# Performance work log

Measured on AMD Instinct MI355X. Metric: run time of the kernel, lower is better.

## Reference

```python
import jax, jax.numpy as jnp
import numpy as np

EMBED_DIM = 1024
NUM_HEADS = 16
HEAD_DIM = EMBED_DIM // NUM_HEADS


def setup_inputs() -> dict:
    key = jax.random.key(0)
    kx, kw1, kb1, kw2, kb2 = jax.random.split(key, 5)
    B, T, C = 4, 2048, EMBED_DIM
    s = 1.0 / np.sqrt(C)
    return {
        "x": jax.random.normal(kx, (B, T, C), dtype=jnp.float32),
        "qkv_w": jax.random.uniform(kw1, (3 * C, C), jnp.float32, -s, s),
        "qkv_b": jax.random.uniform(kb1, (3 * C,), jnp.float32, -s, s),
        "out_w": jax.random.uniform(kw2, (C, C), jnp.float32, -s, s),
        "out_b": jax.random.uniform(kb2, (C,), jnp.float32, -s, s),
    }


def reference(x, qkv_w, qkv_b, out_w, out_b):
    B, T, C = x.shape
    H, D = NUM_HEADS, HEAD_DIM
    qkv = x @ qkv_w.T + qkv_b                      # [B,T,3C]
    qkv = qkv.reshape(B, T, 3, H, D)
    q = qkv[:, :, 0].transpose(0, 2, 1, 3)         # [B,H,T,D]
    k = qkv[:, :, 1].transpose(0, 2, 1, 3)
    v = qkv[:, :, 2].transpose(0, 2, 1, 3)
    att = jnp.einsum("bhqd,bhkd->bhqk", q, k) / jnp.sqrt(jnp.float32(D))
    causal = jnp.tril(jnp.ones((T, T), dtype=bool))
    att = jnp.where(causal, att, -jnp.inf)
    att = jax.nn.softmax(att, axis=-1)
    out = jnp.einsum("bhqk,bhkd->bhqd", att, v)    # [B,H,T,D]
    out = out.transpose(0, 2, 1, 3).reshape(B, T, C)
    return out @ out_w.T + out_b
```

## Files before the change

### kernel.cpp

```cpp
#include <hip/hip_runtime.h>
#include <stdint.h>

typedef _Float16 f16;
typedef _Float16 f16x2 __attribute__((ext_vector_type(2)));
typedef _Float16 f16x4 __attribute__((ext_vector_type(4)));
typedef _Float16 f16x8 __attribute__((ext_vector_type(8)));
typedef float f32x4 __attribute__((ext_vector_type(4)));

#define LOG2E 1.44269504088896340736f

__device__ __forceinline__ f32x4 mfma_16x16x32(f16x8 a, f16x8 b, f32x4 c) {
    return __builtin_amdgcn_mfma_f32_16x16x32_f16(a, b, c, 0, 0, 0);
}

__device__ __forceinline__ void gload_lds16(const void* g, void* l) {
    __builtin_amdgcn_global_load_lds(
        (const __attribute__((address_space(1))) unsigned int*)g,
        (__attribute__((address_space(3))) unsigned int*)l, 16, 0, 0);
}

__device__ __forceinline__ f16x2 cvt_pk_f16(float a, float b) {
    return __builtin_bit_cast(f16x2, __builtin_amdgcn_cvt_pkrtz(a, b));
}

__global__ void cast_f32_f16(const float* __restrict__ src, f16* __restrict__ dst, int n4) {
    int i = blockIdx.x * 256 + threadIdx.x;
    if (i >= n4) return;
    float4 v = reinterpret_cast<const float4*>(src)[i];
    f16x4 o;
    o[0] = (f16)v.x; o[1] = (f16)v.y; o[2] = (f16)v.z; o[3] = (f16)v.w;
    reinterpret_cast<f16x4*>(dst)[i] = o;
}

template<int MODE>
__global__ __launch_bounds__(256, 2)
void gemm_tn(const f16* __restrict__ A, const f16* __restrict__ W,
             const float* __restrict__ bias, void* __restrict__ outp,
             int M, int N, int K)
{
    __shared__ __align__(16) f16 As[128 * 32];
    __shared__ __align__(16) f16 Bs[128 * 32];

    const int lane = threadIdx.x & 63;
    const int wave = threadIdx.x >> 6;
    const int l15 = lane & 15, l4 = lane >> 4;

    const int nwg = (int)(gridDim.x * gridDim.y);
    int orig = (int)(blockIdx.y * gridDim.x + blockIdx.x);
    int cpx = nwg >> 3;
    int w = (orig & 7) * cpx + (orig >> 3);
    const int row0 = (w / (int)gridDim.x) * 128;
    const int col0 = (w % (int)gridDim.x) * 128;
    const int wr = wave >> 1, wc = wave & 1;

    f32x4 acc[4][4] = {};

    const int srow = lane >> 2;
    const int scol = (lane & 3) * 8;

    for (int k0 = 0; k0 < K; k0 += 32) {
        __syncthreads();
        #pragma unroll
        for (int it = 0; it < 2; ++it) {
            int chunk = it * 4 + wave;
            const f16* gA = A + (size_t)(row0 + chunk * 16 + srow) * K + k0 + scol;
            gload_lds16(gA, As + chunk * 512);
            const f16* gB = W + (size_t)(col0 + chunk * 16 + srow) * K + k0 + scol;
            gload_lds16(gB, Bs + chunk * 512);
        }
        __syncthreads();

        f16x8 af[4], bf[4];
        #pragma unroll
        for (int m = 0; m < 4; ++m)
            af[m] = *reinterpret_cast<const f16x8*>(As + (wr * 64 + m * 16 + l15) * 32 + l4 * 8);
        #pragma unroll
        for (int n = 0; n < 4; ++n)
            bf[n] = *reinterpret_cast<const f16x8*>(Bs + (wc * 64 + n * 16 + l15) * 32 + l4 * 8);
        #pragma unroll
        for (int m = 0; m < 4; ++m)
            #pragma unroll
            for (int n = 0; n < 4; ++n)
                acc[m][n] = mfma_16x16x32(af[m], bf[n], acc[m][n]);
    }

    if (MODE == 0) {
        f16* qb = (f16*)outp;
        const size_t HS = (size_t)64 * 2048 * 64;
        #pragma unroll
        for (int m = 0; m < 4; ++m) {
            int rbase = row0 + wr * 64 + m * 16 + l4 * 4;
            #pragma unroll
            for (int n = 0; n < 4; ++n) {
                int j = col0 + wc * 64 + n * 16 + l15;
                int which = j >> 10;
                int h = (j >> 6) & 15;
                int d = j & 63;
                float bj = bias[j];
                f16* base = qb + (size_t)which * HS;
                float scale = (which == 0) ? (0.125f * LOG2E) : 1.0f;
                #pragma unroll
                for (int r = 0; r < 4; ++r) {
                    int row = rbase + r;
                    int b = row >> 11, t = row & 2047;
                    size_t off = ((size_t)(b * 16 + h) * 2048 + t) * 64 + d;
                    base[off] = (f16)((acc[m][n][r] + bj) * scale);
                }
            }
        }
    } else {
        float* O = (float*)outp;
        #pragma unroll
        for (int m = 0; m < 4; ++m) {
            int rbase = row0 + wr * 64 + m * 16 + l4 * 4;
            #pragma unroll
            for (int n = 0; n < 4; ++n) {
                int j = col0 + wc * 64 + n * 16 + l15;
                float bj = bias[j];
                #pragma unroll
                for (int r = 0; r < 4; ++r)
                    O[(size_t)(rbase + r) * N + j] = acc[m][n][r] + bj;
            }
        }
    }
}

__global__ __launch_bounds__(256, 3)
void attn_kernel(const f16* __restrict__ qb, const f16* __restrict__ kb,
                 const f16* __restrict__ vb, f16* __restrict__ ob)
{
    __shared__ __align__(16) f16 Ks[2][64 * 64];
    __shared__ __align__(16) f16 Vs[2][64][72];
    __shared__ __align__(16) f16 Ps[4][16][72];

    const int tid = (int)threadIdx.x;
    const int bh = (int)blockIdx.x;
    const int qblk = (int)gridDim.y - 1 - (int)blockIdx.y;
    const int lane = tid & 63;
    const int wave = tid >> 6;
    const int l15 = lane & 15, l4 = lane >> 4;
    const int q0 = qblk * 64;
    const int qw = q0 + wave * 16;

    const f16* Qp = qb + ((size_t)bh * 2048 + qw) * 64;
    f16x8 aq0 = *reinterpret_cast<const f16x8*>(Qp + l15 * 64 + l4 * 8);
    f16x8 aq1 = *reinterpret_cast<const f16x8*>(Qp + l15 * 64 + 32 + l4 * 8);

    float Mr = -1e30f, Lr = 0.0f;
    f32x4 oacc[4] = {};

    const int ntiles = q0 / 64 + 1;
    const f16* Kbh = kb + (size_t)bh * 2048 * 64;
    const f16* Vbh = vb + (size_t)bh * 2048 * 64;

    f16x8 vld0, vld1;
    {
        #pragma unroll
        for (int it = 0; it < 2; ++it) {
            int c = it * 256 + tid;
            int krow = c >> 3;
            int s16 = (c & 7) ^ (krow & 7);
            gload_lds16(Kbh + krow * 64 + s16 * 8, &Ks[0][0] + it * 2048 + wave * 512);
        }
        vld0 = *reinterpret_cast<const f16x8*>(Vbh + lane * 64 + (wave * 2 + 0) * 8);
        vld1 = *reinterpret_cast<const f16x8*>(Vbh + lane * 64 + (wave * 2 + 1) * 8);
    }

    for (int t = 0; t < ntiles; ++t) {
        const int cur = t & 1;

        #pragma unroll
        for (int it = 0; it < 2; ++it) {
            int dblk = wave * 2 + it;
            const f16x8 v = it ? vld1 : vld0;
            #pragma unroll
            for (int e = 0; e < 8; ++e)
                Vs[cur][dblk * 8 + e][lane] = v[e];
        }

        __syncthreads();

        {
            const int kvn = (t + 1 < ntiles) ? (t + 1) * 64 : t * 64;
            const f16* Ktn = Kbh + (size_t)kvn * 64;
            #pragma unroll
            for (int it = 0; it < 2; ++it) {
                int c = it * 256 + tid;
                int krow = c >> 3;
                int s16 = (c & 7) ^ (krow & 7);
                gload_lds16(Ktn + krow * 64 + s16 * 8, &Ks[cur ^ 1][0] + it * 2048 + wave * 512);
            }
            const f16* Vtn = Vbh + (size_t)kvn * 64;
            vld0 = *reinterpret_cast<const f16x8*>(Vtn + lane * 64 + (wave * 2 + 0) * 8);
            vld1 = *reinterpret_cast<const f16x8*>(Vtn + lane * 64 + (wave * 2 + 1) * 8);
        }

        f32x4 s[4];
        __builtin_amdgcn_s_setprio(1);
        #pragma unroll
        for (int n = 0; n < 4; ++n) {
            int key = n * 16 + l15;
            int cs = key & 7;
            f16x8 kf0 = *reinterpret_cast<const f16x8*>(&Ks[cur][0] + key * 64 + ((l4 ^ cs) * 8));
            f16x8 kf1 = *reinterpret_cast<const f16x8*>(&Ks[cur][0] + key * 64 + (((4 + l4) ^ cs) * 8));
            f32x4 c = {};
            c = mfma_16x16x32(kf0, aq0, c);
            c = mfma_16x16x32(kf1, aq1, c);
            s[n] = c;
        }
        __builtin_amdgcn_s_setprio(0);

        if (t == ntiles - 1) {
            #pragma unroll
            for (int n = 0; n < 4; ++n)
                #pragma unroll
                for (int r = 0; r < 4; ++r)
                    if (n * 16 + l4 * 4 + r > wave * 16 + l15) s[n][r] = -1e30f;
        }

        float mx = -1e30f;
        #pragma unroll
        for (int n = 0; n < 4; ++n)
            #pragma unroll
            for (int r = 0; r < 4; ++r)
                mx = fmaxf(mx, s[n][r]);
        mx = fmaxf(mx, __shfl_xor(mx, 16));
        mx = fmaxf(mx, __shfl_xor(mx, 32));

        if (__any(mx > Mr + 8.0f)) {
            float nm = fmaxf(Mr, mx);
            float alpha = exp2f(Mr - nm);
            Mr = nm;
            float ar[4];
            #pragma unroll
            for (int r = 0; r < 4; ++r) ar[r] = __shfl(alpha, l4 * 4 + r);
            #pragma unroll
            for (int dt = 0; dt < 4; ++dt) {
                oacc[dt][0] *= ar[0]; oacc[dt][1] *= ar[1];
                oacc[dt][2] *= ar[2]; oacc[dt][3] *= ar[3];
            }
            Lr *= alpha;
        }

        float rs = 0.0f;
        #pragma unroll
        for (int n = 0; n < 4; ++n) {
            float p0 = exp2f(s[n][0] - Mr);
            float p1 = exp2f(s[n][1] - Mr);
            float p2 = exp2f(s[n][2] - Mr);
            float p3 = exp2f(s[n][3] - Mr);
            rs += (p0 + p1) + (p2 + p3);
            f16x2 lo = cvt_pk_f16(p0, p1);
            f16x2 hi = cvt_pk_f16(p2, p3);
            f16x4 pk; pk[0] = lo[0]; pk[1] = lo[1]; pk[2] = hi[0]; pk[3] = hi[1];
            *reinterpret_cast<f16x4*>(&Ps[wave][l15][n * 16 + l4 * 4]) = pk;
        }
        rs += __shfl_xor(rs, 16);
        rs += __shfl_xor(rs, 32);
        Lr += rs;

        f16x8 pa0 = *reinterpret_cast<const f16x8*>(&Ps[wave][l15][l4 * 8]);
        f16x8 pa1 = *reinterpret_cast<const f16x8*>(&Ps[wave][l15][32 + l4 * 8]);
        __builtin_amdgcn_s_setprio(1);
        #pragma unroll
        for (int dt = 0; dt < 4; ++dt) {
            int d = dt * 16 + l15;
            f16x8 v0 = *reinterpret_cast<const f16x8*>(&Vs[cur][d][l4 * 8]);
            f16x8 v1 = *reinterpret_cast<const f16x8*>(&Vs[cur][d][32 + l4 * 8]);
            oacc[dt] = mfma_16x16x32(pa0, v0, oacc[dt]);
            oacc[dt] = mfma_16x16x32(pa1, v1, oacc[dt]);
        }
        __builtin_amdgcn_s_setprio(0);
    }

    float lr[4];
    #pragma unroll
    for (int r = 0; r < 4; ++r) lr[r] = __shfl(Lr, l4 * 4 + r);

    const int b = bh >> 4, h = bh & 15;
    f16* O = ob + ((size_t)b * 2048 + qw) * 1024 + h * 64;
    #pragma unroll
    for (int dt = 0; dt < 4; ++dt) {
        int d = dt * 16 + l15;
        #pragma unroll
        for (int r = 0; r < 4; ++r)
            O[(size_t)(l4 * 4 + r) * 1024 + d] = (f16)(oacc[dt][r] / lr[r]);
    }
}

extern "C" void kernel_launch(void* const* d_in, const int* in_sizes, int n_in,
                              void* d_out, int out_size, void* d_ws, size_t ws_size,
                              hipStream_t stream)
{
    const float* x    = (const float*)d_in[0];
    const float* qkvw = (const float*)d_in[1];
    const float* qkvb = (const float*)d_in[2];
    const float* outw = (const float*)d_in[3];
    const float* outb = (const float*)d_in[4];
    float* out = (float*)d_out;

    f16* x_h    = (f16*)d_ws;
    f16* qkvw_h = x_h + (size_t)8192 * 1024;
    f16* outw_h = qkvw_h + (size_t)3072 * 1024;
    f16* q_buf  = outw_h + (size_t)1024 * 1024;
    f16* att_o  = q_buf + (size_t)3 * 8388608;

    cast_f32_f16<<<8192, 256, 0, stream>>>(x, x_h, 2097152);
    cast_f32_f16<<<3072, 256, 0, stream>>>(qkvw, qkvw_h, 786432);
    cast_f32_f16<<<1024, 256, 0, stream>>>(outw, outw_h, 262144);

    gemm_tn<0><<<dim3(24, 64), 256, 0, stream>>>(x_h, qkvw_h, qkvb, q_buf, 8192, 3072, 1024);
    attn_kernel<<<dim3(64, 32), 256, 0, stream>>>(q_buf, q_buf + 8388608, q_buf + 2 * 8388608, att_o);
    gemm_tn<1><<<dim3(8, 64), 256, 0, stream>>>(att_o, outw_h, outb, out, 8192, 1024, 1024);
}
```

Baseline: 198.3 us.

## Use 32x32 MFMA with 128-query tiles in causal attention kernel

The attention kernel now handles 128 query rows per block (32 per wave) with 32x32x16 MFMA tiles in place of 16x16x32. Each K/V tile loaded into LDS is therefore reused by twice as many queries, and the grid shrinks to half as many blocks. Waves whose queries lie entirely before a K/V tile skip its compute, and the K LDS layout changes to a chunked, unswizzled arrangement. The costs are fewer blocks for occupancy, more registers for the 16-wide accumulators, and possible LDS bank conflicts from the new padding.

```diff
diff --git a/kernel.cpp b/kernel.cpp
--- a/kernel.cpp
+++ b/kernel.cpp
@@ -6,11 +6,15 @@
 typedef _Float16 f16x4 __attribute__((ext_vector_type(4)));
 typedef _Float16 f16x8 __attribute__((ext_vector_type(8)));
 typedef float f32x4 __attribute__((ext_vector_type(4)));
+typedef float f32x16 __attribute__((ext_vector_type(16)));
 
 #define LOG2E 1.44269504088896340736f
 
 __device__ __forceinline__ f32x4 mfma_16x16x32(f16x8 a, f16x8 b, f32x4 c) {
     return __builtin_amdgcn_mfma_f32_16x16x32_f16(a, b, c, 0, 0, 0);
+}
+__device__ __forceinline__ f32x16 mfma_32x32x16(f16x8 a, f16x8 b, f32x16 c) {
+    return __builtin_amdgcn_mfma_f32_32x32x16_f16(a, b, c, 0, 0, 0);
 }
 
 __device__ __forceinline__ void gload_lds16(const void* g, void* l) {
@@ -129,27 +133,30 @@
 void attn_kernel(const f16* __restrict__ qb, const f16* __restrict__ kb,
                  const f16* __restrict__ vb, f16* __restrict__ ob)
 {
-    __shared__ __align__(16) f16 Ks[2][64 * 64];
-    __shared__ __align__(16) f16 Vs[2][64][72];
-    __shared__ __align__(16) f16 Ps[4][16][72];
+    __shared__ __align__(16) f16 Ks[2][4096];
+    __shared__ __align__(16) f16 Vs[2][64][68];
+    __shared__ __align__(16) f16 Ps[4][32][68];
 
     const int tid = (int)threadIdx.x;
     const int bh = (int)blockIdx.x;
     const int qblk = (int)gridDim.y - 1 - (int)blockIdx.y;
     const int lane = tid & 63;
     const int wave = tid >> 6;
-    const int l15 = lane & 15, l4 = lane >> 4;
-    const int q0 = qblk * 64;
-    const int qw = q0 + wave * 16;
+    const int l31 = lane & 31;
+    const int hi  = lane >> 5;
+    const int q0 = qblk * 128;
+    const int qw = q0 + wave * 32;
 
     const f16* Qp = qb + ((size_t)bh * 2048 + qw) * 64;
-    f16x8 aq0 = *reinterpret_cast<const f16x8*>(Qp + l15 * 64 + l4 * 8);
-    f16x8 aq1 = *reinterpret_cast<const f16x8*>(Qp + l15 * 64 + 32 + l4 * 8);
+    f16x8 qf[4];
+    #pragma unroll
+    for (int ss = 0; ss < 4; ++ss)
+        qf[ss] = *reinterpret_cast<const f16x8*>(Qp + l31 * 64 + ss * 16 + hi * 8);
 
     float Mr = -1e30f, Lr = 0.0f;
-    f32x4 oacc[4] = {};
-
-    const int ntiles = q0 / 64 + 1;
+    f32x16 oacc[2] = {};
+
+    const int ntiles = 2 * qblk + 2;
     const f16* Kbh = kb + (size_t)bh * 2048 * 64;
     const f16* Vbh = vb + (size_t)bh * 2048 * 64;
 
@@ -157,10 +164,8 @@
     {
         #pragma unroll
         for (int it = 0; it < 2; ++it) {
-            int c = it * 256 + tid;
-            int krow = c >> 3;
-            int s16 = (c & 7) ^ (krow & 7);
-            gload_lds16(Kbh + krow * 64 + s16 * 8, &Ks[0][0] + it * 2048 + wave * 512);
+            int c = it * 4 + wave;
+            gload_lds16(Kbh + lane * 64 + c * 8, &Ks[0][0] + c * 512);
         }
         vld0 = *reinterpret_cast<const f16x8*>(Vbh + lane * 64 + (wave * 2 + 0) * 8);
         vld1 = *reinterpret_cast<const f16x8*>(Vbh + lane * 64 + (wave * 2 + 1) * 8);
@@ -168,6 +173,7 @@
 
     for (int t = 0; t < ntiles; ++t) {
         const int cur = t & 1;
+        const int kv0 = t * 64;
 
         #pragma unroll
         for (int it = 0; it < 2; ++it) {
@@ -185,107 +191,124 @@
             const f16* Ktn = Kbh + (size_t)kvn * 64;
             #pragma unroll
             for (int it = 0; it < 2; ++it) {
-                int c = it * 256 + tid;
-                int krow = c >> 3;
-                int s16 = (c & 7) ^ (krow & 7);
-                gload_lds16(Ktn + krow * 64 + s16 * 8, &Ks[cur ^ 1][0] + it * 2048 + wave * 512);
+                int c = it * 4 + wave;
+                gload_lds16(Ktn + lane * 64 + c * 8, &Ks[cur ^ 1][0] + c * 512);
             }
             const f16* Vtn = Vbh + (size_t)kvn * 64;
             vld0 = *reinterpret_cast<const f16x8*>(Vtn + lane * 64 + (wave * 2 + 0) * 8);
             vld1 = *reinterpret_cast<const f16x8*>(Vtn + lane * 64 + (wave * 2 + 1) * 8);
         }
 
-        f32x4 s[4];
-        __builtin_amdgcn_s_setprio(1);
-        #pragma unroll
-        for (int n = 0; n < 4; ++n) {
-            int key = n * 16 + l15;
-            int cs = key & 7;
-            f16x8 kf0 = *reinterpret_cast<const f16x8*>(&Ks[cur][0] + key * 64 + ((l4 ^ cs) * 8));
-            f16x8 kf1 = *reinterpret_cast<const f16x8*>(&Ks[cur][0] + key * 64 + (((4 + l4) ^ cs) * 8));
-            f32x4 c = {};
-            c = mfma_16x16x32(kf0, aq0, c);
-            c = mfma_16x16x32(kf1, aq1, c);
-            s[n] = c;
-        }
-        __builtin_amdgcn_s_setprio(0);
-
-        if (t == ntiles - 1) {
-            #pragma unroll
-            for (int n = 0; n < 4; ++n)
-                #pragma unroll
-                for (int r = 0; r < 4; ++r)
-                    if (n * 16 + l4 * 4 + r > wave * 16 + l15) s[n][r] = -1e30f;
-        }
-
-        float mx = -1e30f;
-        #pragma unroll
-        for (int n = 0; n < 4; ++n)
-            #pragma unroll
-            for (int r = 0; r < 4; ++r)
-                mx = fmaxf(mx, s[n][r]);
-        mx = fmaxf(mx, __shfl_xor(mx, 16));
-        mx = fmaxf(mx, __shfl_xor(mx, 32));
-
-        if (__any(mx > Mr + 8.0f)) {
-            float nm = fmaxf(Mr, mx);
-            float alpha = exp2f(Mr - nm);
-            Mr = nm;
-            float ar[4];
-            #pragma unroll
-            for (int r = 0; r < 4; ++r) ar[r] = __shfl(alpha, l4 * 4 + r);
-            #pragma unroll
-            for (int dt = 0; dt < 4; ++dt) {
-                oacc[dt][0] *= ar[0]; oacc[dt][1] *= ar[1];
-                oacc[dt][2] *= ar[2]; oacc[dt][3] *= ar[3];
-            }
-            Lr *= alpha;
-        }
-
-        float rs = 0.0f;
-        #pragma unroll
-        for (int n = 0; n < 4; ++n) {
-            float p0 = exp2f(s[n][0] - Mr);
-            float p1 = exp2f(s[n][1] - Mr);
-            float p2 = exp2f(s[n][2] - Mr);
-            float p3 = exp2f(s[n][3] - Mr);
-            rs += (p0 + p1) + (p2 + p3);
-            f16x2 lo = cvt_pk_f16(p0, p1);
-            f16x2 hi = cvt_pk_f16(p2, p3);
-            f16x4 pk; pk[0] = lo[0]; pk[1] = lo[1]; pk[2] = hi[0]; pk[3] = hi[1];
-            *reinterpret_cast<f16x4*>(&Ps[wave][l15][n * 16 + l4 * 4]) = pk;
-        }
-        rs += __shfl_xor(rs, 16);
-        rs += __shfl_xor(rs, 32);
-        Lr += rs;
-
-        f16x8 pa0 = *reinterpret_cast<const f16x8*>(&Ps[wave][l15][l4 * 8]);
-        f16x8 pa1 = *reinterpret_cast<const f16x8*>(&Ps[wave][l15][32 + l4 * 8]);
-        __builtin_amdgcn_s_setprio(1);
-        #pragma unroll
-        for (int dt = 0; dt < 4; ++dt) {
-            int d = dt * 16 + l15;
-            f16x8 v0 = *reinterpret_cast<const f16x8*>(&Vs[cur][d][l4 * 8]);
-            f16x8 v1 = *reinterpret_cast<const f16x8*>(&Vs[cur][d][32 + l4 * 8]);
-            oacc[dt] = mfma_16x16x32(pa0, v0, oacc[dt]);
-            oacc[dt] = mfma_16x16x32(pa1, v1, oacc[dt]);
-        }
-        __builtin_amdgcn_s_setprio(0);
+        if (kv0 <= qw + 31) {
+            const f16* Ksc = &Ks[cur][0];
+
+            f32x16 s0 = {}, s1 = {};
+            __builtin_amdgcn_s_setprio(1);
+            #pragma unroll
+            for (int ss = 0; ss < 4; ++ss) {
+                f16x8 kf0 = *reinterpret_cast<const f16x8*>(Ksc + (2 * ss + hi) * 512 + l31 * 8);
+                f16x8 kf1 = *reinterpret_cast<const f16x8*>(Ksc + (2 * ss + hi) * 512 + (32 + l31) * 8);
+                s0 = mfma_32x32x16(kf0, qf[ss], s0);
+                s1 = mfma_32x32x16(kf1, qf[ss], s1);
+            }
+            __builtin_amdgcn_s_setprio(0);
+
+            if (kv0 + 63 > qw) {
+                const int qg = qw + l31;
+                #pragma unroll
+                for (int r = 0; r < 16; ++r) {
+                    int k0g = kv0 + (r & 3) + 8 * (r >> 2) + 4 * hi;
+                    if (k0g > qg)      s0[r] = -1e30f;
+                    if (k0g + 32 > qg) s1[r] = -1e30f;
+                }
+            }
+
+            float t16[16];
+            #pragma unroll
+            for (int i = 0; i < 16; ++i) t16[i] = fmaxf(s0[i], s1[i]);
+            #pragma unroll
+            for (int st = 8; st > 0; st >>= 1)
+                #pragma unroll
+                for (int i = 0; i < st; ++i) t16[i] = fmaxf(t16[i], t16[i + st]);
+            float mx = t16[0];
+            mx = fmaxf(mx, __shfl_xor(mx, 32));
+
+            if (__any(mx > Mr + 8.0f)) {
+                float nm = fmaxf(Mr, mx);
+                float alpha = exp2f(Mr - nm);
+                Mr = nm; Lr *= alpha;
+                float ar[16];
+                #pragma unroll
+                for (int r = 0; r < 16; ++r)
+                    ar[r] = __shfl(alpha, (r & 3) + 8 * (r >> 2) + 4 * hi);
+                #pragma unroll
+                for (int r = 0; r < 16; ++r) { oacc[0][r] *= ar[r]; oacc[1][r] *= ar[r]; }
+            }
+
+            float e0[16], e1[16];
+            #pragma unroll
+            for (int r = 0; r < 16; ++r) {
+                e0[r] = exp2f(s0[r] - Mr);
+                e1[r] = exp2f(s1[r] - Mr);
+            }
+            float sm[16];
+            #pragma unroll
+            for (int i = 0; i < 16; ++i) sm[i] = e0[i] + e1[i];
+            #pragma unroll
+            for (int st = 8; st > 0; st >>= 1)
+                #pragma unroll
+                for (int i = 0; i < st; ++i) sm[i] += sm[i + st];
+            float rs = sm[0];
+            rs += __shfl_xor(rs, 32);
+            Lr += rs;
+
+            f16* Pw = &Ps[wave][l31][0];
+            #pragma unroll
+            for (int w = 0; w < 4; ++w) {
+                f16x2 lo0 = cvt_pk_f16(e0[4 * w],     e0[4 * w + 1]);
+                f16x2 hi0 = cvt_pk_f16(e0[4 * w + 2], e0[4 * w + 3]);
+                f16x4 p4; p4[0] = lo0[0]; p4[1] = lo0[1]; p4[2] = hi0[0]; p4[3] = hi0[1];
+                *reinterpret_cast<f16x4*>(Pw + 8 * w + 4 * hi) = p4;
+                f16x2 lo1 = cvt_pk_f16(e1[4 * w],     e1[4 * w + 1]);
+                f16x2 hi1 = cvt_pk_f16(e1[4 * w + 2], e1[4 * w + 3]);
+                f16x4 q4; q4[0] = lo1[0]; q4[1] = lo1[1]; q4[2] = hi1[0]; q4[3] = hi1[1];
+                *reinterpret_cast<f16x4*>(Pw + 32 + 8 * w + 4 * hi) = q4;
+            }
+
+            __builtin_amdgcn_s_setprio(1);
+            #pragma unroll
+            for (int ss = 0; ss < 4; ++ss) {
+                f16x4 a0 = *reinterpret_cast<const f16x4*>(Pw + 16 * ss + 8 * hi);
+                f16x4 a1 = *reinterpret_cast<const f16x4*>(Pw + 16 * ss + 8 * hi + 4);
+                f16x8 pa = __builtin_shufflevector(a0, a1, 0, 1, 2, 3, 4, 5, 6, 7);
+                #pragma unroll
+                for (int db = 0; db < 2; ++db) {
+                    const f16* vp = &Vs[cur][db * 32 + l31][16 * ss + 8 * hi];
+                    f16x4 v0 = *reinterpret_cast<const f16x4*>(vp);
+                    f16x4 v1 = *reinterpret_cast<const f16x4*>(vp + 4);
+                    f16x8 vf = __builtin_shufflevector(v0, v1, 0, 1, 2, 3, 4, 5, 6, 7);
+                    oacc[db] = mfma_32x32x16(pa, vf, oacc[db]);
+                }
+            }
+            __builtin_amdgcn_s_setprio(0);
+        }
     }
 
-    float lr[4];
+    float rcp = 1.0f / Lr;
+    float rr[16];
     #pragma unroll
-    for (int r = 0; r < 4; ++r) lr[r] = __shfl(Lr, l4 * 4 + r);
+    for (int r = 0; r < 16; ++r)
+        rr[r] = __shfl(rcp, (r & 3) + 8 * (r >> 2) + 4 * hi);
 
     const int b = bh >> 4, h = bh & 15;
     f16* O = ob + ((size_t)b * 2048 + qw) * 1024 + h * 64;
     #pragma unroll
-    for (int dt = 0; dt < 4; ++dt) {
-        int d = dt * 16 + l15;
-        #pragma unroll
-        for (int r = 0; r < 4; ++r)
-            O[(size_t)(l4 * 4 + r) * 1024 + d] = (f16)(oacc[dt][r] / lr[r]);
-    }
+    for (int db = 0; db < 2; ++db)
+        #pragma unroll
+        for (int r = 0; r < 16; ++r) {
+            int q = (r & 3) + 8 * (r >> 2) + 4 * hi;
+            O[(size_t)q * 1024 + db * 32 + l31] = (f16)(oacc[db][r] * rr[r]);
+        }
 }
 
 extern "C" void kernel_launch(void* const* d_in, const int* in_sizes, int n_in,
@@ -310,6 +333,6 @@
     cast_f32_f16<<<1024, 256, 0, stream>>>(outw, outw_h, 262144);
 
     gemm_tn<0><<<dim3(24, 64), 256, 0, stream>>>(x_h, qkvw_h, qkvb, q_buf, 8192, 3072, 1024);
-    attn_kernel<<<dim3(64, 32), 256, 0, stream>>>(q_buf, q_buf + 8388608, q_buf + 2 * 8388608, att_o);
+    attn_kernel<<<dim3(64, 16), 256, 0, stream>>>(q_buf, q_buf + 8388608, q_buf + 2 * 8388608, att_o);
     gemm_tn<1><<<dim3(8, 64), 256, 0, stream>>>(att_o, outw_h, outb, out, 8192, 1024, 1024);
 }
```

Result: faster. 191.1 us (-3.6%).
